# Performance work log

Hardware: AMD Instinct MI355X
Metric: run time of the kernel (lower is better)

Reference implementation:

```python
import jax, jax.numpy as jnp
import numpy as np

LN_EPS = 1e-5

def _layernorm(z, g, b):
    m = jnp.mean(z, axis=-1, keepdims=True)
    v = jnp.mean(jnp.square(z - m), axis=-1, keepdims=True)
    return (z - m) / jnp.sqrt(v + LN_EPS) * g + b

def setup_inputs() -> dict:
    key = jax.random.key(0)
    ks = jax.random.split(key, 8)
    B, N, C, H = 16, 1024, 384, 6
    Dff = 4 * C
    s = 0.02
    return {
        "x": jax.random.normal(ks[0], (B, N, C), dtype=jnp.float32),
        "ln1_g": jnp.ones((C,), jnp.float32),
        "ln1_b": jnp.zeros((C,), jnp.float32),
        "qkv_w": jax.random.normal(ks[1], (3 * C, C), jnp.float32) * s,
        "proj_w": jax.random.normal(ks[2], (C, C), jnp.float32) * s,
        "proj_b": jnp.zeros((C,), jnp.float32),
        "gate_h": jnp.ones((H,), jnp.float32),
        "ln2_g": jnp.ones((C,), jnp.float32),
        "ln2_b": jnp.zeros((C,), jnp.float32),
        "fc1_w": jax.random.normal(ks[3], (Dff, C), jnp.float32) * s,
        "fc1_b": jnp.zeros((Dff,), jnp.float32),
        "fc2_w": jax.random.normal(ks[4], (C, Dff), jnp.float32) * s,
        "fc2_b": jnp.zeros((C,), jnp.float32),
        "gate_mlp": jnp.ones((Dff,), jnp.float32),
    }

def reference(x, ln1_g, ln1_b, qkv_w, proj_w, proj_b, gate_h,
              ln2_g, ln2_b, fc1_w, fc1_b, fc2_w, fc2_b, gate_mlp):
    B, N, C = x.shape
    H = gate_h.shape[0]
    Dh = C // H
    scale = Dh ** -0.5

    # Attention branch
    h = _layernorm(x, ln1_g, ln1_b)
    qkv = (h @ qkv_w.T).reshape(B, N, 3, H, Dh).transpose(2, 0, 3, 1, 4)  # [3,B,H,N,Dh]
    q, k, v = qkv[0], qkv[1], qkv[2]
    attn = jax.nn.softmax(jnp.einsum('bhnd,bhmd->bhnm', q, k) * scale, axis=-1)  # [B,H,N,N]
    o = jnp.einsum('bhnm,bhmd->bhnd', attn, v)            # [B,H,N,Dh]
    o = o.transpose(0, 2, 1, 3) * gate_h[None, None, :, None]  # per-head gate
    o = o.reshape(B, N, C) @ proj_w.T + proj_b
    x = x + o

    # MLP branch (exact GELU, per-neuron gate)
    h2 = _layernorm(x, ln2_g, ln2_b)
    m = jax.nn.gelu(h2 @ fc1_w.T + fc1_b, approximate=False) * gate_mlp
    x = x + (m @ fc2_w.T + fc2_b)
    return x
```

## Files before the change

### kernel.cpp

```cpp
#include <hip/hip_runtime.h>
#include <hip/hip_bf16.h>
#include <cstdint>
#include <cstddef>

#define B_   16
#define N_   1024
#define C_   384
#define H_   6
#define DFF_ 1536
#define R_   16384

typedef __attribute__((ext_vector_type(8))) __bf16 bf16x8;
typedef __attribute__((ext_vector_type(4))) float  f32x4;
typedef __attribute__((ext_vector_type(8))) unsigned short u16x8;
typedef __attribute__((ext_vector_type(4))) unsigned short u16x4;

__device__ __forceinline__ float bf2f(unsigned short u){
    unsigned int x = ((unsigned int)u) << 16;
    return __builtin_bit_cast(float, x);
}
__device__ __forceinline__ unsigned short f2bf(float f){
    return __builtin_bit_cast(unsigned short, __float2bfloat16(f));
}
__device__ __forceinline__ unsigned int cvt_pk_bf16(float a, float b){
    unsigned int r;
    asm("v_cvt_pk_bf16_f32 %0, %1, %2" : "=v"(r) : "v"(a), "v"(b));
    return r;
}
__device__ __forceinline__ float fast_exp2(float x){
    float r;
    asm("v_exp_f32 %0, %1" : "=v"(r) : "v"(x));
    return r;
}
__device__ __forceinline__ void gload16(const void* g, void* l){
    __builtin_amdgcn_global_load_lds(
        (const __attribute__((address_space(1))) unsigned int*)g,
        (__attribute__((address_space(3))) unsigned int*)l, 16, 0, 0);
}
__device__ __forceinline__ float gelu_f(float u){
    float z  = fabsf(u) * 0.70710678118654752f;
    float t  = __builtin_amdgcn_rcpf(1.0f + 0.47047f*z);
    float e  = __expf(-z*z);
    float p  = t*(0.3480242f + t*(-0.0958798f + t*0.7478556f));
    float er = 1.0f - p*e;
    return 0.5f*u*(1.0f + copysignf(er, u));
}
__device__ __forceinline__ float ldv(const float* p, size_t i){ return p[i]; }
__device__ __forceinline__ float ldv(const __hip_bfloat16* p, size_t i){ return __bfloat162float(p[i]); }

__global__ __launch_bounds__(256) void ln1_cvt_kernel(
    const float* __restrict__ x, const float* __restrict__ g,
    const float* __restrict__ b, __hip_bfloat16* __restrict__ out,
    const float* __restrict__ i0, __hip_bfloat16* __restrict__ o0, int n0,
    const float* __restrict__ i1, __hip_bfloat16* __restrict__ o1, int n1,
    const float* __restrict__ i2, __hip_bfloat16* __restrict__ o2, int n2,
    const float* __restrict__ i3, __hip_bfloat16* __restrict__ o3, int n3)
{
    if (blockIdx.x < 4096){
        const int lane = threadIdx.x & 63;
        const int wave = threadIdx.x >> 6;
        const int row  = blockIdx.x*4 + wave;
        const float* xr = x + (size_t)row*C_;
        float v[6];
        float s = 0.f;
        #pragma unroll
        for (int i=0;i<6;i++){ v[i] = xr[lane + i*64]; s += v[i]; }
        #pragma unroll
        for (int m=1;m<64;m<<=1) s += __shfl_xor(s, m);
        const float mean = s * (1.0f/C_);
        float sq = 0.f;
        #pragma unroll
        for (int i=0;i<6;i++){ float d = v[i]-mean; sq += d*d; }
        #pragma unroll
        for (int m=1;m<64;m<<=1) sq += __shfl_xor(sq, m);
        const float rstd = rsqrtf(sq*(1.0f/C_) + 1e-5f);
        #pragma unroll
        for (int i=0;i<6;i++){
            int c = lane + i*64;
            out[(size_t)row*C_ + c] = __float2bfloat16((v[i]-mean)*rstd*g[c] + b[c]);
        }
    } else {
        const int total = n0+n1+n2+n3;
        for (int i = (blockIdx.x-4096)*blockDim.x + threadIdx.x; i < total; i += 1024*blockDim.x){
            int k = i;
            if (k < n0){ o0[k] = __float2bfloat16(i0[k]); continue; }
            k -= n0;
            if (k < n1){ o1[k] = __float2bfloat16(i1[k]); continue; }
            k -= n1;
            if (k < n2){ o2[k] = __float2bfloat16(i2[k]); continue; }
            k -= n2;
            o3[k] = __float2bfloat16(i3[k]);
        }
    }
}

template<typename T>
__global__ __launch_bounds__(256) void ln_kernel(
    const T* __restrict__ x, const float* __restrict__ g,
    const float* __restrict__ b, __hip_bfloat16* __restrict__ out)
{
    const int lane = threadIdx.x & 63;
    const int wave = threadIdx.x >> 6;
    const int row  = blockIdx.x*4 + wave;
    const T* xr = x + (size_t)row*C_;
    float v[6];
    float s = 0.f;
    #pragma unroll
    for (int i=0;i<6;i++){ v[i] = ldv(xr, lane + i*64); s += v[i]; }
    #pragma unroll
    for (int m=1;m<64;m<<=1) s += __shfl_xor(s, m);
    const float mean = s * (1.0f/C_);
    float sq = 0.f;
    #pragma unroll
    for (int i=0;i<6;i++){ float d = v[i]-mean; sq += d*d; }
    #pragma unroll
    for (int m=1;m<64;m<<=1) sq += __shfl_xor(sq, m);
    const float rstd = rsqrtf(sq*(1.0f/C_) + 1e-5f);
    #pragma unroll
    for (int i=0;i<6;i++){
        int c = lane + i*64;
        out[(size_t)row*C_ + c] = __float2bfloat16((v[i]-mean)*rstd*g[c] + b[c]);
    }
}

#define BK2 32
enum { EPI_QKV=0, EPI_PROJ=1, EPI_FC1=2, EPI_FC2=3 };

template<int EPI, int BMt, int BNt, int NBUF, int MW, int NTH>
__global__ __launch_bounds__(NTH, MW) void gemm_bt(
    const __hip_bfloat16* __restrict__ A,
    const __hip_bfloat16* __restrict__ W,
    const int M, const int N, const int K,
    const float* __restrict__ bias,
    const float* __restrict__ resid,
    const __hip_bfloat16* __restrict__ residb,
    const float* __restrict__ gate,
    float* __restrict__ outf,
    __hip_bfloat16* __restrict__ outb)
{
    constexpr int NWAVE = NTH/64;
    constexpr int NWC   = (BNt >= 128) ? 2 : 1;
    constexpr int NWR   = NWAVE/NWC;
    constexpr int WRS   = BMt/NWR;
    constexpr int MI    = WRS/16;
    constexpr int APASS = (BMt*BK2*2)/(NTH*16);
    constexpr int BPASS = (BNt*BK2*2)/(NTH*16);
    constexpr int LPT   = APASS + BPASS;
    constexpr int RPP   = NTH/4;
    __shared__ __align__(16) unsigned short As[NBUF][BMt*BK2];
    __shared__ __align__(16) unsigned short Bs[NBUF][BNt*BK2];
    const int t = threadIdx.x;
    const int l = t & 63;
    const int w = t >> 6;
    const int wr = (NWC==2) ? (w >> 1) : w;
    const int wc = (NWC==2) ? (w & 1)  : 0;
    const int nb = N / BNt;
    const int rbX = (M/BMt) >> 3;
    const int X  = blockIdx.x & 7;
    const int j8 = blockIdx.x >> 3;
    const int rb = X*rbX + j8 / nb;
    const int cb = j8 % nb;
    const int srow2 = t >> 2;
    const int sgcol = (((t&3) - ((t>>3)&3)) & 3) * 8;
    f32x4 acc[MI][4];
    #pragma unroll
    for (int i=0;i<MI;i++)
        #pragma unroll
        for (int jj=0;jj<4;jj++) acc[i][jj] = (f32x4){0.f,0.f,0.f,0.f};

    const size_t arow0 = (size_t)rb*BMt + srow2;
    const size_t brow0 = (size_t)cb*BNt + srow2;

    auto STAGE = [&](int buf, int k0){
        #pragma unroll
        for (int c=0;c<APASS;c++)
            gload16(A + (arow0 + c*RPP)*K + k0 + sgcol, (char*)&As[buf][0] + c*(NTH*16) + t*16);
        #pragma unroll
        for (int c=0;c<BPASS;c++)
            gload16(W + (brow0 + c*RPP)*K + k0 + sgcol, (char*)&Bs[buf][0] + c*(NTH*16) + t*16);
    };

    auto COMPUTE = [&](int buf){
        const char* as = (const char*)&As[buf][0];
        const char* bs = (const char*)&Bs[buf][0];
        bf16x8 af[MI], bw[4];
        #pragma unroll
        for (int i=0;i<MI;i++){
            const int r = wr*WRS + i*16 + (l&15);
            const int sl = ((l>>4) + ((r>>1)&3)) & 3;
            af[i] = *(const bf16x8*)(as + r*64 + sl*16);
        }
        #pragma unroll
        for (int i=0;i<4;i++){
            const int r = wc*64 + i*16 + (l&15);
            const int sl = ((l>>4) + ((r>>1)&3)) & 3;
            bw[i] = *(const bf16x8*)(bs + r*64 + sl*16);
        }
        #pragma unroll
        for (int mi=0;mi<MI;mi++)
            #pragma unroll
            for (int ni=0;ni<4;ni++)
                acc[mi][ni] = __builtin_amdgcn_mfma_f32_16x16x32_bf16(af[mi], bw[ni], acc[mi][ni], 0,0,0);
    };

    const int nst = K/BK2;
    if constexpr (NBUF==2){
        STAGE(0, 0);
        for (int s=0; s<nst; ++s){
            asm volatile("s_waitcnt vmcnt(0)" ::: "memory");
            __builtin_amdgcn_s_barrier();
            asm volatile("" ::: "memory");
            if (s+1 < nst) STAGE((s+1)&1, (s+1)*BK2);
            COMPUTE(s&1);
        }
    } else {
        STAGE(0, 0);
        STAGE(1, BK2);
        int cur = 0, stb = 2;
        for (int s=0; s<nst; ++s){
            if (s < nst-1){
                if constexpr (LPT==4) asm volatile("s_waitcnt vmcnt(4)" ::: "memory");
                else                  asm volatile("s_waitcnt vmcnt(3)" ::: "memory");
            } else {
                asm volatile("s_waitcnt vmcnt(0)" ::: "memory");
            }
            __builtin_amdgcn_s_barrier();
            asm volatile("" ::: "memory");
            if (s+2 < nst){
                STAGE(stb, (s+2)*BK2);
                stb = (stb+1==3) ? 0 : stb+1;
            }
            COMPUTE(cur);
            cur = (cur+1==3) ? 0 : cur+1;
        }
    }
    const int rowBase = rb*BMt + wr*WRS;
    const int colBase = cb*BNt + wc*64;
    if constexpr (EPI==EPI_QKV){
        unsigned short* ob = (unsigned short*)outb;
        #pragma unroll
        for (int ni=0; ni<4; ni++){
            const int col = colBase + ni*16 + (l&15);
            const int p = col/384, rem = col - p*384;
            const int hh = rem>>6, d = rem&63;
            #pragma unroll
            for (int mi=0; mi<MI; mi++){
                const int row0 = rowBase + mi*16 + (l>>4)*4;
                const int bb = row0>>10, n = row0&1023;
                if (p==2){
                    u16x4 pk;
                    #pragma unroll
                    for (int jj=0;jj<4;jj++) pk[jj] = f2bf(acc[mi][ni][jj]);
                    *(u16x4*)(ob + (size_t)2*6291456 + ((size_t)(bb*H_+hh)*64 + d)*1024 + n) = pk;
                } else {
                    #pragma unroll
                    for (int jj=0;jj<4;jj++)
                        ob[(((size_t)((p*16+bb)*6+hh))<<16) + ((size_t)(n+jj)<<6) + d] = f2bf(acc[mi][ni][jj]);
                }
            }
        }
    } else {
        #pragma unroll
        for (int ni=0; ni<4; ni++){
            const int col = colBase + ni*16 + (l&15);
            #pragma unroll
            for (int mi=0; mi<MI; mi++){
                #pragma unroll
                for (int jj=0;jj<4;jj++){
                    const int row = rowBase + mi*16 + (l>>4)*4 + jj;
                    const float vx = acc[mi][ni][jj];
                    size_t idx = (size_t)row*N + col;
                    if constexpr (EPI==EPI_PROJ){
                        outb[idx] = __float2bfloat16(resid[idx] + vx + bias[col]);
                    } else if constexpr (EPI==EPI_FC2){
                        outf[idx] = bf2f(*((const unsigned short*)residb + idx)) + vx + bias[col];
                    } else {
                        outb[idx] = __float2bfloat16(gelu_f(vx + bias[col]) * gate[col]);
                    }
                }
            }
        }
    }
}

__global__ __launch_bounds__(256, 2) void gemm_wres_fc1(
    const __hip_bfloat16* __restrict__ A,
    const __hip_bfloat16* __restrict__ Wt,
    const float* __restrict__ bias,
    const float* __restrict__ gate,
    __hip_bfloat16* __restrict__ outb)
{
    __shared__ __align__(16) unsigned short As[3][128*32];
    __shared__ __align__(16) unsigned short Bs[64*384];
    const int t = threadIdx.x;
    const int l = t & 63;
    const int w = t >> 6;
    const int nb = 24;
    const int X  = blockIdx.x & 7;
    const int j8 = blockIdx.x >> 3;
    const int rb = X*16 + j8 / nb;
    const int cb = j8 % nb;

    #pragma unroll
    for (int j=0;j<12;j++){
        const int L   = (w*12 + j)*1024 + l*16;
        const int row = L / 768;
        const int cbyte = L - row*768;
        const int scol  = (cbyte ^ ((row&7)<<4)) >> 1;
        gload16(Wt + (size_t)(cb*64 + row)*384 + scol, (char*)&Bs[0] + L);
    }
    const int sgcol = (((l&3) - ((l>>3)&3)) & 3) * 8;
    const size_t arowW = (size_t)rb*128 + w*32 + (l>>2);
    auto STAGEA = [&](int buf, int s){
        #pragma unroll
        for (int c=0;c<2;c++)
            gload16(A + (arowW + c*16)*384 + s*32 + sgcol,
                    (char*)&As[buf][0] + w*2048 + c*1024 + l*16);
    };
    STAGEA(0, 0);
    STAGEA(1, 1);
    asm volatile("s_waitcnt vmcnt(4)" ::: "memory");
    __builtin_amdgcn_s_barrier();

    f32x4 acc[2][4];
    #pragma unroll
    for (int i=0;i<2;i++)
        #pragma unroll
        for (int jj=0;jj<4;jj++) acc[i][jj] = (f32x4){0.f,0.f,0.f,0.f};

    const char* asbase = (const char*)&As[0][0];
    #pragma unroll
    for (int s=0; s<12; ++s){
        if (s < 11) asm volatile("s_waitcnt vmcnt(2)" ::: "memory");
        else        asm volatile("s_waitcnt vmcnt(0)" ::: "memory");
        const char* as = asbase + (s%3)*8192 + w*2048;
        bf16x8 af[2], bw[4];
        #pragma unroll
        for (int i=0;i<2;i++){
            const int r  = i*16 + (l&15);
            const int sl = ((l>>4) + ((r>>1)&3)) & 3;
            af[i] = *(const bf16x8*)(as + r*64 + sl*16);
        }
        #pragma unroll
        for (int i=0;i<4;i++){
            const int r = i*16 + (l&15);
            bw[i] = *(const bf16x8*)((const char*)&Bs[0] + r*768
                         + ((s*64 + (l>>4)*16) ^ ((r&7)<<4)));
        }
        #pragma unroll
        for (int mi=0;mi<2;mi++)
            #pragma unroll
            for (int ni=0;ni<4;ni++)
                acc[mi][ni] = __builtin_amdgcn_mfma_f32_16x16x32_bf16(af[mi], bw[ni], acc[mi][ni], 0,0,0);
        asm volatile("s_waitcnt lgkmcnt(0)" ::: "memory");
        if (s+2 < 12) STAGEA((s+2)%3, s+2);
    }
    const int rowBase = rb*128 + w*32;
    const int colBase = cb*64;
    #pragma unroll
    for (int ni=0; ni<4; ni++){
        const int col = colBase + ni*16 + (l&15);
        #pragma unroll
        for (int mi=0; mi<2; mi++){
            #pragma unroll
            for (int jj=0;jj<4;jj++){
                const int row = rowBase + mi*16 + (l>>4)*4 + jj;
                outb[(size_t)row*1536 + col] =
                    __float2bfloat16(gelu_f(acc[mi][ni][jj] + bias[col]) * gate[col]);
            }
        }
    }
}

__global__ __launch_bounds__(256) void attn_mfma(
    const __hip_bfloat16* __restrict__ qg,
    const __hip_bfloat16* __restrict__ kg,
    const __hip_bfloat16* __restrict__ vtg,
    const float* __restrict__ gate_h,
    __hip_bfloat16* __restrict__ og)
{
    __shared__ __align__(16) unsigned short Ks [3][64*64];
    __shared__ __align__(16) unsigned short Vts[3][64*64];
    const int t = threadIdx.x;
    const int l = t & 63;
    const int w = t >> 6;
    const int X  = blockIdx.x & 7;
    const int j8 = blockIdx.x >> 3;
    const int bh = X*12 + (j8 >> 3);
    const int n0 = (j8 & 7) * 128;
    const int h  = bh % H_;
    const int b  = bh / H_;
    const unsigned short* qp  = (const unsigned short*)qg  + ((size_t)bh*N_ + n0 + w*32)*64;
    const unsigned short* kp  = (const unsigned short*)kg  + (size_t)bh*N_*64;
    const unsigned short* vtp = (const unsigned short*)vtg + (size_t)bh*64*N_;

    bf16x8 qf[2][2];
    #pragma unroll
    for (int mt=0;mt<2;mt++)
        #pragma unroll
        for (int dc=0;dc<2;dc++){
            u16x8 raw = *(const u16x8*)(qp + ((size_t)(mt*16 + (l&15)))*64 + dc*32 + (l>>4)*8);
            u16x8 sc;
            #pragma unroll
            for (int j=0;j<8;j++) sc[j] = f2bf(bf2f(raw[j]) * 0.1803368801111244f);
            qf[mt][dc] = __builtin_bit_cast(bf16x8, sc);
        }

    int qk_off[4][2], pv_off[2][4];
    #pragma unroll
    for (int t4=0;t4<4;t4++){
        const int i    = l & 15;
        const int row  = 8*(i>>2) + (i&3) + 4*(t4&1) + 32*(t4>>1);
        const int swzr = (row&3) | (((row>>3)&1)<<2);
        #pragma unroll
        for (int dc=0;dc<2;dc++)
            qk_off[t4][dc] = row*128 + ((dc*64 + (l>>4)*16) ^ (swzr<<4));
    }
    #pragma unroll
    for (int nt=0;nt<4;nt++){
        const int row  = nt*16 + (l&15);
        const int swzr = (row&3) | (((row>>3)&1)<<2);
        #pragma unroll
        for (int kc=0;kc<2;kc++)
            pv_off[kc][nt] = row*128 + ((kc*64 + (l>>4)*16) ^ (swzr<<4));
    }

    const int sr  = t >> 3;
    const int sce = (t & 7) * 8;

    auto STAGE = [&](int buf, int kt){
        #pragma unroll
        for (int c=0;c<2;c++){
            const int r    = sr + c*32;
            const int swzr = (r&3) | (((r>>3)&1)<<2);
            const int col  = sce ^ (swzr<<3);
            gload16(kp  + ((size_t)(kt*64 + r))*64 + col, (char*)&Ks [buf][0] + (c*256 + t)*16);
            gload16(vtp + (size_t)r*N_ + kt*64 + col,     (char*)&Vts[buf][0] + (c*256 + t)*16);
        }
    };

    f32x4 o_acc[2][4];
    #pragma unroll
    for (int i=0;i<2;i++)
        #pragma unroll
        for (int jj=0;jj<4;jj++) o_acc[i][jj] = (f32x4){0.f,0.f,0.f,0.f};
    float rs_part[2] = {0.f, 0.f};

    STAGE(0, 0);
    STAGE(1, 1);
    int cur = 0, stb = 2;
    for (int kt=0; kt<16; kt++){
        if (kt < 15) asm volatile("s_waitcnt vmcnt(4)" ::: "memory");
        else         asm volatile("s_waitcnt vmcnt(0)" ::: "memory");
        __builtin_amdgcn_s_barrier();
        asm volatile("" ::: "memory");
        if (kt < 14){
            STAGE(stb, kt+2);
            stb = (stb+1==3) ? 0 : stb+1;
        }
        const char* ks = (const char*)&Ks[cur][0];
        const char* vs = (const char*)&Vts[cur][0];

        f32x4 s_acc[4][2];
        #pragma unroll
        for (int i=0;i<4;i++)
            #pragma unroll
            for (int jj=0;jj<2;jj++) s_acc[i][jj] = (f32x4){0.f,0.f,0.f,0.f};
        #pragma unroll
        for (int t4=0;t4<4;t4++)
            #pragma unroll
            for (int dc=0;dc<2;dc++){
                bf16x8 kf = *(const bf16x8*)(ks + qk_off[t4][dc]);
                #pragma unroll
                for (int mt=0;mt<2;mt++)
                    s_acc[t4][mt] = __builtin_amdgcn_mfma_f32_16x16x32_bf16(kf, qf[mt][dc], s_acc[t4][mt], 0,0,0);
            }
        #pragma unroll
        for (int mt=0;mt<2;mt++){
            float acc_s = 0.f;
            #pragma unroll
            for (int t4=0;t4<4;t4++){
                #pragma unroll
                for (int jj=0;jj<4;jj++){
                    float e = fast_exp2(s_acc[t4][mt][jj]);
                    s_acc[t4][mt][jj] = e;
                    acc_s += e;
                }
            }
            rs_part[mt] += acc_s;
        }
        #pragma unroll
        for (int kc=0;kc<2;kc++){
            union { unsigned int u[4]; bf16x8 v; } pu[2];
            #pragma unroll
            for (int mt=0;mt<2;mt++){
                pu[mt].u[0] = cvt_pk_bf16(s_acc[2*kc  ][mt][0], s_acc[2*kc  ][mt][1]);
                pu[mt].u[1] = cvt_pk_bf16(s_acc[2*kc  ][mt][2], s_acc[2*kc  ][mt][3]);
                pu[mt].u[2] = cvt_pk_bf16(s_acc[2*kc+1][mt][0], s_acc[2*kc+1][mt][1]);
                pu[mt].u[3] = cvt_pk_bf16(s_acc[2*kc+1][mt][2], s_acc[2*kc+1][mt][3]);
            }
            #pragma unroll
            for (int nt=0;nt<4;nt++){
                bf16x8 vf = *(const bf16x8*)(vs + pv_off[kc][nt]);
                #pragma unroll
                for (int mt=0;mt<2;mt++)
                    o_acc[mt][nt] = __builtin_amdgcn_mfma_f32_16x16x32_bf16(pu[mt].v, vf, o_acc[mt][nt], 0,0,0);
            }
        }
        cur = (cur+1==3) ? 0 : cur+1;
    }
    float rowsum[2];
    #pragma unroll
    for (int mt=0;mt<2;mt++){
        float rs = rs_part[mt];
        rs += __shfl_xor(rs, 16);
        rs += __shfl_xor(rs, 32);
        rowsum[mt] = rs;
    }
    const float gh = gate_h[h];
    float inv[2][4];
    #pragma unroll
    for (int mt=0;mt<2;mt++)
        #pragma unroll
        for (int r=0;r<4;r++)
            inv[mt][r] = gh / __shfl(rowsum[mt], (l>>4)*4 + r, 16);
    unsigned short* op = (unsigned short*)og + ((size_t)b*N_ + n0 + w*32)*C_ + h*64;
    #pragma unroll
    for (int mt=0;mt<2;mt++){
        #pragma unroll
        for (int r=0;r<4;r++){
            const int n = mt*16 + (l>>4)*4 + r;
            #pragma unroll
            for (int nt=0;nt<4;nt++)
                op[(size_t)n*C_ + nt*16 + (l&15)] = f2bf(o_acc[mt][nt][r]*inv[mt][r]);
        }
    }
}

extern "C" void kernel_launch(void* const* d_in, const int* in_sizes, int n_in,
                              void* d_out, int out_size, void* d_ws, size_t ws_size,
                              hipStream_t stream)
{
    const float* x     = (const float*)d_in[0];
    const float* ln1g  = (const float*)d_in[1];
    const float* ln1b  = (const float*)d_in[2];
    const float* qkvw  = (const float*)d_in[3];
    const float* projw = (const float*)d_in[4];
    const float* projb = (const float*)d_in[5];
    const float* gateh = (const float*)d_in[6];
    const float* ln2g  = (const float*)d_in[7];
    const float* ln2b  = (const float*)d_in[8];
    const float* fc1w  = (const float*)d_in[9];
    const float* fc1b  = (const float*)d_in[10];
    const float* fc2w  = (const float*)d_in[11];
    const float* fc2b  = (const float*)d_in[12];
    const float* gatem = (const float*)d_in[13];
    float* out = (float*)d_out;

    char* ws = (char*)d_ws;
    __hip_bfloat16* h_buf = (__hip_bfloat16*)(ws + 0);
    __hip_bfloat16* qkv   = (__hip_bfloat16*)(ws + 12582912);
    __hip_bfloat16* q_buf = qkv;
    __hip_bfloat16* k_buf = qkv + 6291456;
    __hip_bfloat16* vt_buf= qkv + 2*6291456;
    __hip_bfloat16* o_buf = (__hip_bfloat16*)(ws + 50331648);
    __hip_bfloat16* m_buf = (__hip_bfloat16*)(ws + 12582912);
    __hip_bfloat16* x1b   = (__hip_bfloat16*)(ws + 62914560);
    __hip_bfloat16* wqkv  = (__hip_bfloat16*)(ws + 88080384);
    __hip_bfloat16* wproj = (__hip_bfloat16*)(ws + 88965120);
    __hip_bfloat16* wfc1  = (__hip_bfloat16*)(ws + 89260032);
    __hip_bfloat16* wfc2  = (__hip_bfloat16*)(ws + 90439680);

    ln1_cvt_kernel<<<5120, 256, 0, stream>>>(x, ln1g, ln1b, h_buf,
                                             qkvw, wqkv, 1152*384,
                                             projw, wproj, 384*384,
                                             fc1w, wfc1, 1536*384,
                                             fc2w, wfc2, 384*1536);

    gemm_bt<EPI_QKV,128,128,3,3,256><<<1152, 256, 0, stream>>>(h_buf, wqkv, R_, 1152, 384,
                                                               nullptr, nullptr, nullptr, nullptr, nullptr, qkv);
    attn_mfma<<<768, 256, 0, stream>>>(q_buf, k_buf, vt_buf, gateh, o_buf);
    gemm_bt<EPI_PROJ,64,128,3,1,256><<<768, 256, 0, stream>>>(o_buf, wproj, R_, 384, 384,
                                                              projb, x, nullptr, nullptr, nullptr, x1b);
    ln_kernel<__hip_bfloat16><<<4096, 256, 0, stream>>>(x1b, ln2g, ln2b, h_buf);
    gemm_wres_fc1<<<3072, 256, 0, stream>>>(h_buf, wfc1, fc1b, gatem, m_buf);
    gemm_bt<EPI_FC2,64,128,3,1,256><<<768, 256, 0, stream>>>(m_buf, wfc2, R_, 384, 1536,
                                                             fc2b, nullptr, x1b, nullptr, out, nullptr);
}
```

Baseline: 177.9 us.

## Generalize weight-resident GEMM and reuse it for QKV, proj and FC1 with two row tiles

Turns the FC1-only weight-resident GEMM into a template with QKV, proj and FC1 epilogues. Each block now keeps its 64x384 weight slice in LDS and handles two 128-row tiles, which halves the block count and amortizes the weight load. A/activation staging goes from 3 to 4 buffers with a prefetch distance of 3 that runs across both row tiles. QKV and proj move off the generic tiled GEMM onto this kernel, trading their larger tiles for weight reuse and possibly lower occupancy per block.

```diff
diff --git a/kernel.cpp b/kernel.cpp
--- a/kernel.cpp
+++ b/kernel.cpp
@@ -236,137 +236,147 @@
     }
     const int rowBase = rb*BMt + wr*WRS;
     const int colBase = cb*BNt + wc*64;
-    if constexpr (EPI==EPI_QKV){
-        unsigned short* ob = (unsigned short*)outb;
-        #pragma unroll
-        for (int ni=0; ni<4; ni++){
-            const int col = colBase + ni*16 + (l&15);
-            const int p = col/384, rem = col - p*384;
-            const int hh = rem>>6, d = rem&63;
-            #pragma unroll
-            for (int mi=0; mi<MI; mi++){
-                const int row0 = rowBase + mi*16 + (l>>4)*4;
-                const int bb = row0>>10, n = row0&1023;
-                if (p==2){
-                    u16x4 pk;
-                    #pragma unroll
-                    for (int jj=0;jj<4;jj++) pk[jj] = f2bf(acc[mi][ni][jj]);
-                    *(u16x4*)(ob + (size_t)2*6291456 + ((size_t)(bb*H_+hh)*64 + d)*1024 + n) = pk;
+    #pragma unroll
+    for (int ni=0; ni<4; ni++){
+        const int col = colBase + ni*16 + (l&15);
+        #pragma unroll
+        for (int mi=0; mi<MI; mi++){
+            #pragma unroll
+            for (int jj=0;jj<4;jj++){
+                const int row = rowBase + mi*16 + (l>>4)*4 + jj;
+                const float vx = acc[mi][ni][jj];
+                size_t idx = (size_t)row*N + col;
+                if constexpr (EPI==EPI_PROJ){
+                    outb[idx] = __float2bfloat16(resid[idx] + vx + bias[col]);
+                } else if constexpr (EPI==EPI_FC2){
+                    outf[idx] = bf2f(*((const unsigned short*)residb + idx)) + vx + bias[col];
                 } else {
-                    #pragma unroll
-                    for (int jj=0;jj<4;jj++)
-                        ob[(((size_t)((p*16+bb)*6+hh))<<16) + ((size_t)(n+jj)<<6) + d] = f2bf(acc[mi][ni][jj]);
+                    outb[idx] = __float2bfloat16(gelu_f(vx + bias[col]) * gate[col]);
                 }
             }
         }
-    } else {
-        #pragma unroll
-        for (int ni=0; ni<4; ni++){
-            const int col = colBase + ni*16 + (l&15);
-            #pragma unroll
-            for (int mi=0; mi<MI; mi++){
-                #pragma unroll
-                for (int jj=0;jj<4;jj++){
-                    const int row = rowBase + mi*16 + (l>>4)*4 + jj;
-                    const float vx = acc[mi][ni][jj];
-                    size_t idx = (size_t)row*N + col;
-                    if constexpr (EPI==EPI_PROJ){
-                        outb[idx] = __float2bfloat16(resid[idx] + vx + bias[col]);
-                    } else if constexpr (EPI==EPI_FC2){
-                        outf[idx] = bf2f(*((const unsigned short*)residb + idx)) + vx + bias[col];
-                    } else {
-                        outb[idx] = __float2bfloat16(gelu_f(vx + bias[col]) * gate[col]);
-                    }
-                }
-            }
-        }
-    }
-}
-
-__global__ __launch_bounds__(256, 2) void gemm_wres_fc1(
+    }
+}
+
+template<int EPI, int NCOLS>
+__global__ __launch_bounds__(256, 2) void gemm_wres(
     const __hip_bfloat16* __restrict__ A,
     const __hip_bfloat16* __restrict__ Wt,
     const float* __restrict__ bias,
+    const float* __restrict__ resid,
     const float* __restrict__ gate,
     __hip_bfloat16* __restrict__ outb)
 {
-    __shared__ __align__(16) unsigned short As[3][128*32];
+    constexpr int NB = NCOLS/64;
+    constexpr int G  = 24;
+    __shared__ __align__(16) unsigned short As[4][128*32];
     __shared__ __align__(16) unsigned short Bs[64*384];
     const int t = threadIdx.x;
     const int l = t & 63;
     const int w = t >> 6;
-    const int nb = 24;
     const int X  = blockIdx.x & 7;
     const int j8 = blockIdx.x >> 3;
-    const int rb = X*16 + j8 / nb;
-    const int cb = j8 % nb;
+    const int rb = X*8 + j8 / NB;
+    const int cb = j8 % NB;
 
     #pragma unroll
     for (int j=0;j<12;j++){
-        const int L   = (w*12 + j)*1024 + l*16;
-        const int row = L / 768;
+        const int L     = (w*12 + j)*1024 + l*16;
+        const int row   = L / 768;
         const int cbyte = L - row*768;
         const int scol  = (cbyte ^ ((row&7)<<4)) >> 1;
         gload16(Wt + (size_t)(cb*64 + row)*384 + scol, (char*)&Bs[0] + L);
     }
     const int sgcol = (((l&3) - ((l>>3)&3)) & 3) * 8;
-    const size_t arowW = (size_t)rb*128 + w*32 + (l>>2);
-    auto STAGEA = [&](int buf, int s){
+    const size_t arow0 = (size_t)rb*256 + w*32 + (l>>2);
+    auto STAGEA = [&](int g){
+        const int rt = g/12, s = g - rt*12;
         #pragma unroll
         for (int c=0;c<2;c++)
-            gload16(A + (arowW + c*16)*384 + s*32 + sgcol,
-                    (char*)&As[buf][0] + w*2048 + c*1024 + l*16);
+            gload16(A + (arow0 + rt*128 + c*16)*384 + s*32 + sgcol,
+                    (char*)&As[g&3][0] + w*2048 + c*1024 + l*16);
     };
-    STAGEA(0, 0);
-    STAGEA(1, 1);
-    asm volatile("s_waitcnt vmcnt(4)" ::: "memory");
+    STAGEA(0); STAGEA(1); STAGEA(2);
+    asm volatile("s_waitcnt vmcnt(6)" ::: "memory");
     __builtin_amdgcn_s_barrier();
 
-    f32x4 acc[2][4];
-    #pragma unroll
-    for (int i=0;i<2;i++)
-        #pragma unroll
-        for (int jj=0;jj<4;jj++) acc[i][jj] = (f32x4){0.f,0.f,0.f,0.f};
-
-    const char* asbase = (const char*)&As[0][0];
-    #pragma unroll
-    for (int s=0; s<12; ++s){
-        if (s < 11) asm volatile("s_waitcnt vmcnt(2)" ::: "memory");
-        else        asm volatile("s_waitcnt vmcnt(0)" ::: "memory");
-        const char* as = asbase + (s%3)*8192 + w*2048;
-        bf16x8 af[2], bw[4];
-        #pragma unroll
-        for (int i=0;i<2;i++){
-            const int r  = i*16 + (l&15);
-            const int sl = ((l>>4) + ((r>>1)&3)) & 3;
-            af[i] = *(const bf16x8*)(as + r*64 + sl*16);
-        }
-        #pragma unroll
-        for (int i=0;i<4;i++){
-            const int r = i*16 + (l&15);
-            bw[i] = *(const bf16x8*)((const char*)&Bs[0] + r*768
-                         + ((s*64 + (l>>4)*16) ^ ((r&7)<<4)));
-        }
-        #pragma unroll
-        for (int mi=0;mi<2;mi++)
-            #pragma unroll
-            for (int ni=0;ni<4;ni++)
-                acc[mi][ni] = __builtin_amdgcn_mfma_f32_16x16x32_bf16(af[mi], bw[ni], acc[mi][ni], 0,0,0);
-        asm volatile("s_waitcnt lgkmcnt(0)" ::: "memory");
-        if (s+2 < 12) STAGEA((s+2)%3, s+2);
-    }
-    const int rowBase = rb*128 + w*32;
-    const int colBase = cb*64;
-    #pragma unroll
-    for (int ni=0; ni<4; ni++){
-        const int col = colBase + ni*16 + (l&15);
-        #pragma unroll
-        for (int mi=0; mi<2; mi++){
-            #pragma unroll
-            for (int jj=0;jj<4;jj++){
-                const int row = rowBase + mi*16 + (l>>4)*4 + jj;
-                outb[(size_t)row*1536 + col] =
-                    __float2bfloat16(gelu_f(acc[mi][ni][jj] + bias[col]) * gate[col]);
+    #pragma unroll
+    for (int rt=0; rt<2; ++rt){
+        f32x4 acc[2][4];
+        #pragma unroll
+        for (int i=0;i<2;i++)
+            #pragma unroll
+            for (int jj=0;jj<4;jj++) acc[i][jj] = (f32x4){0.f,0.f,0.f,0.f};
+
+        #pragma unroll
+        for (int s=0; s<12; ++s){
+            const int g = rt*12 + s;
+            if (g <= G-3)      asm volatile("s_waitcnt vmcnt(4)" ::: "memory");
+            else if (g == G-2) asm volatile("s_waitcnt vmcnt(2)" ::: "memory");
+            else               asm volatile("s_waitcnt vmcnt(0)" ::: "memory");
+            const char* as = (const char*)&As[g&3][0] + w*2048;
+            bf16x8 af[2], bw[4];
+            #pragma unroll
+            for (int i=0;i<2;i++){
+                const int r  = i*16 + (l&15);
+                const int sl = ((l>>4) + ((r>>1)&3)) & 3;
+                af[i] = *(const bf16x8*)(as + r*64 + sl*16);
+            }
+            #pragma unroll
+            for (int i=0;i<4;i++){
+                const int r = i*16 + (l&15);
+                bw[i] = *(const bf16x8*)((const char*)&Bs[0] + r*768
+                             + ((s*64 + (l>>4)*16) ^ ((r&7)<<4)));
+            }
+            #pragma unroll
+            for (int mi=0;mi<2;mi++)
+                #pragma unroll
+                for (int ni=0;ni<4;ni++)
+                    acc[mi][ni] = __builtin_amdgcn_mfma_f32_16x16x32_bf16(af[mi], bw[ni], acc[mi][ni], 0,0,0);
+            asm volatile("s_waitcnt lgkmcnt(0)" ::: "memory");
+            if (g+3 < G) STAGEA(g+3);
+        }
+        const int rowBase = rb*256 + rt*128 + w*32;
+        if constexpr (EPI==EPI_QKV){
+            unsigned short* ob = (unsigned short*)outb;
+            #pragma unroll
+            for (int ni=0; ni<4; ni++){
+                const int col = cb*64 + ni*16 + (l&15);
+                const int p = col/384, rem = col - p*384;
+                const int hh = rem>>6, d = rem&63;
+                #pragma unroll
+                for (int mi=0; mi<2; mi++){
+                    const int row0 = rowBase + mi*16 + (l>>4)*4;
+                    const int bb = row0>>10, n = row0&1023;
+                    if (p==2){
+                        u16x4 pk;
+                        #pragma unroll
+                        for (int jj=0;jj<4;jj++) pk[jj] = f2bf(acc[mi][ni][jj]);
+                        *(u16x4*)(ob + (size_t)2*6291456 + ((size_t)(bb*H_+hh)*64 + d)*1024 + n) = pk;
+                    } else {
+                        #pragma unroll
+                        for (int jj=0;jj<4;jj++)
+                            ob[(((size_t)((p*16+bb)*6+hh))<<16) + ((size_t)(n+jj)<<6) + d] = f2bf(acc[mi][ni][jj]);
+                    }
+                }
+            }
+        } else {
+            #pragma unroll
+            for (int ni=0; ni<4; ni++){
+                const int col = cb*64 + ni*16 + (l&15);
+                #pragma unroll
+                for (int mi=0; mi<2; mi++){
+                    #pragma unroll
+                    for (int jj=0;jj<4;jj++){
+                        const int row = rowBase + mi*16 + (l>>4)*4 + jj;
+                        const size_t idx = (size_t)row*NCOLS + col;
+                        if constexpr (EPI==EPI_PROJ){
+                            outb[idx] = __float2bfloat16(resid[idx] + acc[mi][ni][jj] + bias[col]);
+                        } else {
+                            outb[idx] = __float2bfloat16(gelu_f(acc[mi][ni][jj] + bias[col]) * gate[col]);
+                        }
+                    }
+                }
             }
         }
     }
@@ -577,13 +587,11 @@
                                              fc1w, wfc1, 1536*384,
                                              fc2w, wfc2, 384*1536);
 
-    gemm_bt<EPI_QKV,128,128,3,3,256><<<1152, 256, 0, stream>>>(h_buf, wqkv, R_, 1152, 384,
-                                                               nullptr, nullptr, nullptr, nullptr, nullptr, qkv);
+    gemm_wres<EPI_QKV,1152><<<1152, 256, 0, stream>>>(h_buf, wqkv, nullptr, nullptr, nullptr, qkv);
     attn_mfma<<<768, 256, 0, stream>>>(q_buf, k_buf, vt_buf, gateh, o_buf);
-    gemm_bt<EPI_PROJ,64,128,3,1,256><<<768, 256, 0, stream>>>(o_buf, wproj, R_, 384, 384,
-                                                              projb, x, nullptr, nullptr, nullptr, x1b);
+    gemm_wres<EPI_PROJ,384><<<384, 256, 0, stream>>>(o_buf, wproj, projb, x, nullptr, x1b);
     ln_kernel<__hip_bfloat16><<<4096, 256, 0, stream>>>(x1b, ln2g, ln2b, h_buf);
-    gemm_wres_fc1<<<3072, 256, 0, stream>>>(h_buf, wfc1, fc1b, gatem, m_buf);
+    gemm_wres<EPI_FC1,1536><<<1536, 256, 0, stream>>>(h_buf, wfc1, fc1b, nullptr, gatem, m_buf);
     gemm_bt<EPI_FC2,64,128,3,1,256><<<768, 256, 0, stream>>>(m_buf, wfc2, R_, 384, 1536,
                                                              fc2b, nullptr, x1b, nullptr, out, nullptr);
 }
```

Result: faster. 171.0 us (-3.8%).
